# Optimization experiments

Hardware: AMD Instinct MI355X
Metric: run time of the kernel (lower is better)

Reference implementation:

```python
import jax, jax.numpy as jnp
import numpy as np

TGT, BSZ, E = 256, 8, 256
SRC = 4096
H = 8
HD = E // H


def setup_inputs() -> dict:
    key = jax.random.key(0)
    ks = jax.random.split(key, 6)
    return {
        "query": jax.random.normal(ks[0], (TGT, BSZ, E), dtype=jnp.float32),
        "key": jax.random.normal(ks[1], (SRC, BSZ, E), dtype=jnp.float32),
        "value": jax.random.normal(ks[2], (SRC, BSZ, E), dtype=jnp.float32),
        "proposal_mask": jax.random.uniform(ks[3], (BSZ, TGT, SRC), dtype=jnp.float32),
        "out_proj_weight": jax.random.normal(ks[4], (E, E), dtype=jnp.float32) * (1.0 / np.sqrt(E)),
        "out_proj_bias": jax.random.normal(ks[5], (E,), dtype=jnp.float32) * 0.01,
    }


def reference(query, key, value, proposal_mask, out_proj_weight, out_proj_bias):
    tgt_len, bsz, embed_dim = query.shape
    src_len = key.shape[0]
    num_heads = H
    head_dim = embed_dim // num_heads

    # v: (src, bsz, E) -> (src, bsz*H, hd) -> (bsz*H, src, hd); index q = b*H + h
    v = value.reshape(src_len, bsz * num_heads, head_dim).transpose(1, 0, 2)

    # proposal_mask (bsz, tgt, src); torch loop+stack produces mask_nhead[b*H+h] = proposal_mask[b]
    mask_nhead = jnp.repeat(proposal_mask, num_heads, axis=0)  # (bsz*H, tgt, src)

    # weighted sum of values per head (no score compute)
    attn_output = jnp.einsum('qts,qsc->qtc', mask_nhead, v)  # (bsz*H, tgt, hd)

    # (bsz*H, tgt, hd) -> (tgt, bsz*H, hd) -> (tgt, bsz, E)
    attn_output = attn_output.transpose(1, 0, 2).reshape(tgt_len, bsz, embed_dim)

    # out projection (outDecoderLayer=False)
    attn_output = attn_output @ out_proj_weight.T + out_proj_bias

    # averaged weights: mask repeated per head -> mean over heads == proposal_mask
    attn_weights = mask_nhead.reshape(bsz, num_heads, tgt_len, src_len).sum(axis=1) / num_heads
    return attn_output, attn_weights
```

## Files before the change

kernel.cpp:

```cpp
#include <hip/hip_runtime.h>
#include <hip/hip_bf16.h>

#define TGT 256
#define BSZ 8
#define E   256
#define SRC 4096

typedef __attribute__((ext_vector_type(8))) short           bf16x8;
typedef __attribute__((ext_vector_type(4))) float           f32x4;
typedef __attribute__((ext_vector_type(4))) float           f4;
typedef __attribute__((ext_vector_type(8))) unsigned short  u16x8;
typedef __attribute__((ext_vector_type(4))) unsigned short  u16x4;

__device__ inline unsigned short f2b(float x) {
    union { __hip_bfloat16 h; unsigned short u; } cv;
    cv.h = __float2bfloat16(x);
    return cv.u;
}

__device__ inline bf16x8 cvt8v(const float* __restrict__ p) {
    f4 lo = *(const f4*)p;
    f4 hi = *(const f4*)(p + 4);
    bf16x8 r;
    #pragma unroll
    for (int j = 0; j < 4; ++j) { r[j] = (short)f2b(lo[j]); r[4 + j] = (short)f2b(hi[j]); }
    return r;
}

__global__ __launch_bounds__(128) void prep_w(
    const float* __restrict__ wgt, unsigned short* __restrict__ wf)
{
    int o    = blockIdx.x * 128 + threadIdx.x;
    int et   = o >> 9;
    int ks   = (o >> 6) & 7;
    int lane = o & 63;
    int quad = lane >> 4, l15 = lane & 15;
    bf16x8 v = cvt8v(wgt + (size_t)(et * 16 + l15) * E + ks * 32 + quad * 8);
    *(bf16x8*)&wf[(size_t)o * 8] = v;
}

__global__ __launch_bounds__(256, 4) void prep_vw(
    const float* __restrict__ value, const unsigned short* __restrict__ wf,
    const float* __restrict__ bias,
    unsigned short* __restrict__ vwf, float* __restrict__ out0)
{
    const int tid = threadIdx.x;

    if (blockIdx.y == 8) {
        #pragma unroll
        for (int s = 0; s < 4; ++s) {
            int f4i = s * 32768 + blockIdx.x * 256 + tid;
            *(f4*)(out0 + (size_t)f4i * 4) = *(const f4*)(bias + (f4i & 63) * 4);
        }
        return;
    }

    __shared__ unsigned short tile[32 * 264];
    const int sc32 = blockIdx.x;
    const int b    = blockIdx.y;
    const int s0   = sc32 * 32;

    #pragma unroll
    for (int i = 0; i < 8; ++i) {
        int lin = i * 256 + tid;
        int row = lin >> 6;
        int c4  = lin & 63;
        f4 v = *(const f4*)(value + (size_t)(s0 + row) * (BSZ * E)
                                  + (size_t)b * E + c4 * 4);
        u16x4 pk;
        #pragma unroll
        for (int j = 0; j < 4; ++j) pk[j] = f2b(v[j]);
        *(u16x4*)&tile[row * 264 + c4 * 4] = pk;
    }
    __syncthreads();

    const int w    = tid >> 6;
    const int lane = tid & 63;
    const int quad = lane >> 4;
    const int l15  = lane & 15;
    const int mt   = w >> 1;
    const int et0  = (w & 1) * 8;

    bf16x8 a[8];
    #pragma unroll
    for (int ks = 0; ks < 8; ++ks)
        a[ks] = *(const bf16x8*)&tile[(mt * 16 + l15) * 264 + ks * 32 + quad * 8];

    const unsigned short* bfw = wf + ((size_t)et0 * 8) * 512 + (size_t)lane * 8;
    f32x4 acc[8] = {};
    #pragma unroll
    for (int ks = 0; ks < 8; ++ks) {
        bf16x8 bb[8];
        #pragma unroll
        for (int e = 0; e < 8; ++e)
            bb[e] = *(const bf16x8*)(bfw + (size_t)(e * 8 + ks) * 512);
        #pragma unroll
        for (int e = 0; e < 8; ++e)
            acc[e] = __builtin_amdgcn_mfma_f32_16x16x32_bf16(a[ks], bb[e], acc[e], 0, 0, 0);
    }

    const int lp = (mt * 2 + (quad >> 1)) * 16 + l15;
    const int j0 = (quad & 1) * 4;
    #pragma unroll
    for (int e = 0; e < 8; ++e) {
        u16x4 pk;
        #pragma unroll
        for (int r = 0; r < 4; ++r) pk[r] = f2b(acc[e][r]);
        *(u16x4*)&vwf[((((size_t)b * 16 + et0 + e) * 128 + sc32) * 64 + lp) * 8 + j0] = pk;
    }
}

#define GP 520

__global__ __launch_bounds__(256, 4) void gemm1(
    const float* __restrict__ mask,
    const unsigned short* __restrict__ vwf,
    float* __restrict__ out1,
    float* __restrict__ out0)
{
    __shared__ unsigned short As[16 * GP];
    const int bx  = blockIdx.x;
    const int b   = bx & 7;
    const int tt  = (bx >> 3) & 15;
    const int kc  = bx >> 7;
    const int t0  = tt * 16;
    const int k0  = kc * 512;
    const int tid = threadIdx.x;
    const int w    = tid >> 6;
    const int lane = tid & 63;
    const int quad = lane >> 4;
    const int l15  = lane & 15;

    const float* mbase = mask + (size_t)b * TGT * SRC + (size_t)t0 * SRC + k0;
    float*       obase = out1 + (size_t)b * TGT * SRC + (size_t)t0 * SRC + k0;

    const int srow = tid >> 4;
    const int sc4  = tid & 15;
    f4 mv[8];
    #pragma unroll
    for (int j = 0; j < 8; ++j)
        mv[j] = __builtin_nontemporal_load(
                    (const f4*)(mbase + (size_t)srow * SRC + (sc4 + j * 16) * 4));
    #pragma unroll
    for (int j = 0; j < 8; ++j) {
        u16x4 pk;
        #pragma unroll
        for (int t = 0; t < 4; ++t) pk[t] = f2b(mv[j][t]);
        *(u16x4*)&As[srow * GP + (sc4 + j * 16) * 4] = pk;
    }
    __syncthreads();

    #pragma unroll
    for (int j = 0; j < 8; ++j)
        __builtin_nontemporal_store(
            mv[j], (f4*)(obase + (size_t)srow * SRC + (sc4 + j * 16) * 4));

    const unsigned short* bfr = vwf + (((size_t)b * 16 + (size_t)w * 4) * 128
                                       + (size_t)kc * 16) * 512 + (size_t)lane * 8;

    f32x4 acc[4] = {};
    #pragma unroll 4
    for (int q = 0; q < 16; ++q) {
        bf16x8 a0 = *(const bf16x8*)&As[l15 * GP + q * 32 + quad * 8];
        bf16x8 B0 = *(const bf16x8*)(bfr + ((size_t)0 * 128 + q) * 512);
        bf16x8 B1 = *(const bf16x8*)(bfr + ((size_t)1 * 128 + q) * 512);
        bf16x8 B2 = *(const bf16x8*)(bfr + ((size_t)2 * 128 + q) * 512);
        bf16x8 B3 = *(const bf16x8*)(bfr + ((size_t)3 * 128 + q) * 512);
        acc[0] = __builtin_amdgcn_mfma_f32_16x16x32_bf16(a0, B0, acc[0], 0, 0, 0);
        acc[1] = __builtin_amdgcn_mfma_f32_16x16x32_bf16(a0, B1, acc[1], 0, 0, 0);
        acc[2] = __builtin_amdgcn_mfma_f32_16x16x32_bf16(a0, B2, acc[2], 0, 0, 0);
        acc[3] = __builtin_amdgcn_mfma_f32_16x16x32_bf16(a0, B3, acc[3], 0, 0, 0);
    }

    #pragma unroll
    for (int e = 0; e < 4; ++e) {
        int ecol = (w * 4 + e) * 16 + l15;
        #pragma unroll
        for (int r = 0; r < 4; ++r) {
            int t = t0 + quad * 4 + r;
            atomicAdd(out0 + (size_t)t * (BSZ * E) + (size_t)b * E + ecol, acc[e][r]);
        }
    }
}

extern "C" void kernel_launch(void* const* d_in, const int* in_sizes, int n_in,
                              void* d_out, int out_size, void* d_ws, size_t ws_size,
                              hipStream_t stream)
{
    const float* value = (const float*)d_in[2];
    const float* mask  = (const float*)d_in[3];
    const float* wgt   = (const float*)d_in[4];
    const float* bias  = (const float*)d_in[5];

    float* out0 = (float*)d_out;
    float* out1 = (float*)d_out + (size_t)TGT * BSZ * E;

    unsigned short* vwf = (unsigned short*)d_ws;
    unsigned short* wf  = vwf + (size_t)BSZ * E * SRC;

    prep_w <<<64, 128, 0, stream>>>(wgt, wf);
    prep_vw<<<dim3(128, 9), 256, 0, stream>>>(value, wf, bias, vwf, out0);
    gemm1  <<<1024, 256, 0, stream>>>(mask, vwf, out1, out0);
}
```

Before: 164.7 us.

## Fuse value-projection into mask GEMM kernel, keeping projected V in LDS

Merges the V·W^T projection and the mask×VW GEMM into one kernel: each block owns a 128-wide source chunk for one batch, projects it into shared memory, then loops over all 16 target tiles, streaming the mask and copying it to out1. This removes the global round trip of the projected-value workspace and one launch. The weight conversion and bias initialisation are merged into a single prep kernel. In exchange, the grid shrinks to 256 blocks of 512 threads with large LDS use, the mask stores lose their nontemporal hints, and each block issues more atomics because the split-K chunk is smaller.

```diff
diff --git a/kernel.cpp b/kernel.cpp
--- a/kernel.cpp
+++ b/kernel.cpp
@@ -9,7 +9,6 @@
 typedef __attribute__((ext_vector_type(8))) short           bf16x8;
 typedef __attribute__((ext_vector_type(4))) float           f32x4;
 typedef __attribute__((ext_vector_type(4))) float           f4;
-typedef __attribute__((ext_vector_type(8))) unsigned short  u16x8;
 typedef __attribute__((ext_vector_type(4))) unsigned short  u16x4;
 
 __device__ inline unsigned short f2b(float x) {
@@ -27,158 +26,148 @@
     return r;
 }
 
-__global__ __launch_bounds__(128) void prep_w(
-    const float* __restrict__ wgt, unsigned short* __restrict__ wf)
-{
-    int o    = blockIdx.x * 128 + threadIdx.x;
-    int et   = o >> 9;
-    int ks   = (o >> 6) & 7;
-    int lane = o & 63;
-    int quad = lane >> 4, l15 = lane & 15;
-    bf16x8 v = cvt8v(wgt + (size_t)(et * 16 + l15) * E + ks * 32 + quad * 8);
-    *(bf16x8*)&wf[(size_t)o * 8] = v;
-}
-
-__global__ __launch_bounds__(256, 4) void prep_vw(
-    const float* __restrict__ value, const unsigned short* __restrict__ wf,
-    const float* __restrict__ bias,
-    unsigned short* __restrict__ vwf, float* __restrict__ out0)
+__global__ __launch_bounds__(128) void prep(
+    const float* __restrict__ wgt, const float* __restrict__ bias,
+    unsigned short* __restrict__ wf, float* __restrict__ out0)
 {
     const int tid = threadIdx.x;
-
-    if (blockIdx.y == 8) {
+    if (blockIdx.x < 64) {
+        int o    = blockIdx.x * 128 + tid;
+        int et   = o >> 9;
+        int ks   = (o >> 6) & 7;
+        int lane = o & 63;
+        int quad = lane >> 4, l15 = lane & 15;
+        *(bf16x8*)&wf[(size_t)o * 8] =
+            cvt8v(wgt + (size_t)(et * 16 + l15) * E + ks * 32 + quad * 8);
+    } else {
+        int bx = blockIdx.x - 64;
         #pragma unroll
-        for (int s = 0; s < 4; ++s) {
-            int f4i = s * 32768 + blockIdx.x * 256 + tid;
+        for (int s = 0; s < 8; ++s) {
+            int f4i = s * 16384 + bx * 128 + tid;
             *(f4*)(out0 + (size_t)f4i * 4) = *(const f4*)(bias + (f4i & 63) * 4);
         }
-        return;
-    }
-
-    __shared__ unsigned short tile[32 * 264];
-    const int sc32 = blockIdx.x;
-    const int b    = blockIdx.y;
-    const int s0   = sc32 * 32;
-
-    #pragma unroll
-    for (int i = 0; i < 8; ++i) {
-        int lin = i * 256 + tid;
-        int row = lin >> 6;
-        int c4  = lin & 63;
-        f4 v = *(const f4*)(value + (size_t)(s0 + row) * (BSZ * E)
-                                  + (size_t)b * E + c4 * 4);
-        u16x4 pk;
-        #pragma unroll
-        for (int j = 0; j < 4; ++j) pk[j] = f2b(v[j]);
-        *(u16x4*)&tile[row * 264 + c4 * 4] = pk;
-    }
-    __syncthreads();
-
-    const int w    = tid >> 6;
-    const int lane = tid & 63;
-    const int quad = lane >> 4;
-    const int l15  = lane & 15;
-    const int mt   = w >> 1;
-    const int et0  = (w & 1) * 8;
-
-    bf16x8 a[8];
-    #pragma unroll
-    for (int ks = 0; ks < 8; ++ks)
-        a[ks] = *(const bf16x8*)&tile[(mt * 16 + l15) * 264 + ks * 32 + quad * 8];
-
-    const unsigned short* bfw = wf + ((size_t)et0 * 8) * 512 + (size_t)lane * 8;
-    f32x4 acc[8] = {};
-    #pragma unroll
-    for (int ks = 0; ks < 8; ++ks) {
-        bf16x8 bb[8];
-        #pragma unroll
-        for (int e = 0; e < 8; ++e)
-            bb[e] = *(const bf16x8*)(bfw + (size_t)(e * 8 + ks) * 512);
-        #pragma unroll
-        for (int e = 0; e < 8; ++e)
-            acc[e] = __builtin_amdgcn_mfma_f32_16x16x32_bf16(a[ks], bb[e], acc[e], 0, 0, 0);
-    }
-
-    const int lp = (mt * 2 + (quad >> 1)) * 16 + l15;
-    const int j0 = (quad & 1) * 4;
-    #pragma unroll
-    for (int e = 0; e < 8; ++e) {
-        u16x4 pk;
-        #pragma unroll
-        for (int r = 0; r < 4; ++r) pk[r] = f2b(acc[e][r]);
-        *(u16x4*)&vwf[((((size_t)b * 16 + et0 + e) * 128 + sc32) * 64 + lp) * 8 + j0] = pk;
     }
 }
 
-#define GP 520
+#define VTP 264
+#define MTP 136
 
-__global__ __launch_bounds__(256, 4) void gemm1(
+__global__ __launch_bounds__(512, 2) void mega(
+    const float* __restrict__ value,
     const float* __restrict__ mask,
-    const unsigned short* __restrict__ vwf,
+    const unsigned short* __restrict__ wf,
     float* __restrict__ out1,
     float* __restrict__ out0)
 {
-    __shared__ unsigned short As[16 * GP];
+    __shared__ unsigned short vt[128 * VTP];
+    __shared__ unsigned short vwB[16 * 4 * 64 * 8];
+
     const int bx  = blockIdx.x;
     const int b   = bx & 7;
-    const int tt  = (bx >> 3) & 15;
-    const int kc  = bx >> 7;
-    const int t0  = tt * 16;
-    const int k0  = kc * 512;
+    const int kc  = bx >> 3;
+    const int k0  = kc * 128;
     const int tid = threadIdx.x;
     const int w    = tid >> 6;
     const int lane = tid & 63;
     const int quad = lane >> 4;
     const int l15  = lane & 15;
 
-    const float* mbase = mask + (size_t)b * TGT * SRC + (size_t)t0 * SRC + k0;
-    float*       obase = out1 + (size_t)b * TGT * SRC + (size_t)t0 * SRC + k0;
-
-    const int srow = tid >> 4;
-    const int sc4  = tid & 15;
-    f4 mv[8];
     #pragma unroll
-    for (int j = 0; j < 8; ++j)
-        mv[j] = __builtin_nontemporal_load(
-                    (const f4*)(mbase + (size_t)srow * SRC + (sc4 + j * 16) * 4));
-    #pragma unroll
-    for (int j = 0; j < 8; ++j) {
+    for (int i = 0; i < 16; ++i) {
+        int lin = i * 512 + tid;
+        int row = lin >> 6;
+        int c4  = lin & 63;
+        f4 v = *(const f4*)(value + (size_t)(k0 + row) * (BSZ * E)
+                                  + (size_t)b * E + c4 * 4);
         u16x4 pk;
         #pragma unroll
-        for (int t = 0; t < 4; ++t) pk[t] = f2b(mv[j][t]);
-        *(u16x4*)&As[srow * GP + (sc4 + j * 16) * 4] = pk;
+        for (int j = 0; j < 4; ++j) pk[j] = f2b(v[j]);
+        *(u16x4*)&vt[row * VTP + c4 * 4] = pk;
     }
     __syncthreads();
 
+    bf16x8 a[8];
     #pragma unroll
-    for (int j = 0; j < 8; ++j)
-        __builtin_nontemporal_store(
-            mv[j], (f4*)(obase + (size_t)srow * SRC + (sc4 + j * 16) * 4));
+    for (int ks = 0; ks < 8; ++ks)
+        a[ks] = *(const bf16x8*)&vt[(w * 16 + l15) * VTP + ks * 32 + quad * 8];
 
-    const unsigned short* bfr = vwf + (((size_t)b * 16 + (size_t)w * 4) * 128
-                                       + (size_t)kc * 16) * 512 + (size_t)lane * 8;
+    {
+        const unsigned short* bfw = wf + (size_t)lane * 8;
+        const int qh = w >> 1;
+        const int lp = ((w & 1) * 2 + (quad >> 1)) * 16 + l15;
+        const int j0 = (quad & 1) * 4;
+        bf16x8 bb[8], nb[8];
+        #pragma unroll
+        for (int ks = 0; ks < 8; ++ks)
+            bb[ks] = *(const bf16x8*)(bfw + (size_t)ks * 512);
+        #pragma unroll
+        for (int et = 0; et < 16; ++et) {
+            if (et < 15) {
+                #pragma unroll
+                for (int ks = 0; ks < 8; ++ks)
+                    nb[ks] = *(const bf16x8*)(bfw + (size_t)((et + 1) * 8 + ks) * 512);
+            }
+            f32x4 acc = {};
+            #pragma unroll
+            for (int ks = 0; ks < 8; ++ks)
+                acc = __builtin_amdgcn_mfma_f32_16x16x32_bf16(a[ks], bb[ks], acc, 0, 0, 0);
+            u16x4 pk;
+            #pragma unroll
+            for (int r = 0; r < 4; ++r) pk[r] = f2b(acc[r]);
+            *(u16x4*)&vwB[(((size_t)et * 4 + qh) * 64 + lp) * 8 + j0] = pk;
+            if (et < 15) {
+                #pragma unroll
+                for (int ks = 0; ks < 8; ++ks) bb[ks] = nb[ks];
+            }
+        }
+    }
+    __syncthreads();
 
-    f32x4 acc[4] = {};
-    #pragma unroll 4
-    for (int q = 0; q < 16; ++q) {
-        bf16x8 a0 = *(const bf16x8*)&As[l15 * GP + q * 32 + quad * 8];
-        bf16x8 B0 = *(const bf16x8*)(bfr + ((size_t)0 * 128 + q) * 512);
-        bf16x8 B1 = *(const bf16x8*)(bfr + ((size_t)1 * 128 + q) * 512);
-        bf16x8 B2 = *(const bf16x8*)(bfr + ((size_t)2 * 128 + q) * 512);
-        bf16x8 B3 = *(const bf16x8*)(bfr + ((size_t)3 * 128 + q) * 512);
-        acc[0] = __builtin_amdgcn_mfma_f32_16x16x32_bf16(a0, B0, acc[0], 0, 0, 0);
-        acc[1] = __builtin_amdgcn_mfma_f32_16x16x32_bf16(a0, B1, acc[1], 0, 0, 0);
-        acc[2] = __builtin_amdgcn_mfma_f32_16x16x32_bf16(a0, B2, acc[2], 0, 0, 0);
-        acc[3] = __builtin_amdgcn_mfma_f32_16x16x32_bf16(a0, B3, acc[3], 0, 0, 0);
-    }
+    unsigned short* mt = &vt[w * (16 * MTP)];
+    #pragma unroll
+    for (int it = 0; it < 2; ++it) {
+        const int tt = w + it * 8;
+        const int t0 = tt * 16;
+        const float* mb = mask + (size_t)b * TGT * SRC + (size_t)t0 * SRC + k0;
+        float*       ob = out1 + (size_t)b * TGT * SRC + (size_t)t0 * SRC + k0;
 
-    #pragma unroll
-    for (int e = 0; e < 4; ++e) {
-        int ecol = (w * 4 + e) * 16 + l15;
+        f4 mv[8];
         #pragma unroll
-        for (int r = 0; r < 4; ++r) {
-            int t = t0 + quad * 4 + r;
-            atomicAdd(out0 + (size_t)t * (BSZ * E) + (size_t)b * E + ecol, acc[e][r]);
+        for (int i = 0; i < 8; ++i) {
+            int idx = i * 64 + lane;
+            int row = idx >> 5, c4 = idx & 31;
+            mv[i] = *(const f4*)(mb + (size_t)row * SRC + c4 * 4);
+        }
+        #pragma unroll
+        for (int i = 0; i < 8; ++i) {
+            int idx = i * 64 + lane;
+            int row = idx >> 5, c4 = idx & 31;
+            u16x4 pk;
+            #pragma unroll
+            for (int j = 0; j < 4; ++j) pk[j] = f2b(mv[i][j]);
+            *(u16x4*)&mt[row * MTP + c4 * 4] = pk;
+            *(f4*)(ob + (size_t)row * SRC + c4 * 4) = mv[i];
+        }
+
+        bf16x8 a4[4];
+        #pragma unroll
+        for (int q = 0; q < 4; ++q)
+            a4[q] = *(const bf16x8*)&mt[l15 * MTP + q * 32 + quad * 8];
+
+        #pragma unroll
+        for (int et = 0; et < 16; ++et) {
+            f32x4 acc = {};
+            #pragma unroll
+            for (int q = 0; q < 4; ++q) {
+                bf16x8 vb = *(const bf16x8*)&vwB[(((size_t)et * 4 + q) * 64 + lane) * 8];
+                acc = __builtin_amdgcn_mfma_f32_16x16x32_bf16(a4[q], vb, acc, 0, 0, 0);
+            }
+            const int ecol = et * 16 + l15;
+            #pragma unroll
+            for (int r = 0; r < 4; ++r) {
+                int t = t0 + quad * 4 + r;
+                atomicAdd(out0 + (size_t)t * (BSZ * E) + (size_t)b * E + ecol, acc[r]);
+            }
         }
     }
 }
@@ -195,10 +184,8 @@
     float* out0 = (float*)d_out;
     float* out1 = (float*)d_out + (size_t)TGT * BSZ * E;
 
-    unsigned short* vwf = (unsigned short*)d_ws;
-    unsigned short* wf  = vwf + (size_t)BSZ * E * SRC;
+    unsigned short* wf = (unsigned short*)d_ws;
 
-    prep_w <<<64, 128, 0, stream>>>(wgt, wf);
-    prep_vw<<<dim3(128, 9), 256, 0, stream>>>(value, wf, bias, vwf, out0);
-    gemm1  <<<1024, 256, 0, stream>>>(mask, vwf, out1, out0);
+    prep<<<192, 128, 0, stream>>>(wgt, bias, wf, out0);
+    mega<<<256, 512, 0, stream>>>(value, mask, wf, out1, out0);
 }
```

After: 181.1 us. 1.1x slower.
